# Optimization experiments

Hardware: AMD Instinct MI355X
Metric: run time of the kernel (lower is better)

The kernel has to match this reference:

```python
import jax, jax.numpy as jnp
import numpy as np

B, C, H, W = 8, 8, 640, 640
M = 16  # max instance ids per image (0 = background)
EPS = 1e-12


def setup_inputs() -> dict:
    key = jax.random.key(0)
    k1, k2, k3, k4, k5 = jax.random.split(key, 5)
    outputs = jax.random.normal(k1, (B, C, H, W), dtype=jnp.float32)
    gt_texts = jax.random.randint(k2, (B, H, W), 0, M)
    gt_kernels = jax.random.randint(k3, (B, H, W), 0, M)
    gt_tops = jax.random.randint(k4, (B, H, W), 0, M)
    gt_bots = jax.random.randint(k5, (B, H, W), 0, M)
    return dict(outputs=outputs, gt_texts=gt_texts, gt_kernels=gt_kernels,
                gt_tops=gt_tops, gt_bots=gt_bots)


def _pull_push(outputs, gt_texts, gt_kernels):
    b = outputs.shape[0]
    n = outputs.shape[2] * outputs.shape[3]
    # similarity embedding per pixel: [B, N, 4]
    sim = outputs[:, 4:].reshape(b, 4, n).transpose(0, 2, 1)
    kt = gt_kernels.reshape(b, n)
    tt = gt_texts.reshape(b, n)
    off = jnp.arange(b, dtype=kt.dtype)[:, None] * M
    ids_k = (kt + off).reshape(-1)
    ids_t = (tt + off).reshape(-1)
    sim_flat = sim.reshape(b * n, 4)
    ones = jnp.ones((b * n,), sim.dtype)

    # per-instance kernel centroids G (segment mean over kernel pixels)
    sum_k = jax.ops.segment_sum(sim_flat, ids_k, num_segments=b * M).reshape(b, M, 4)
    cnt_k = jax.ops.segment_sum(ones, ids_k, num_segments=b * M).reshape(b, M)
    G = sum_k / jnp.maximum(cnt_k, 1.0)[..., None]  # [B, M, 4]
    # instance valid iff it has kernel pixels and idx >= 1 (0 is background)
    valid = (cnt_k > 0) & (jnp.arange(M)[None, :] >= 1)

    # pull loss: per text pixel, distance to its instance's kernel centroid
    G_pix = jnp.take_along_axis(G, tt[..., None], axis=1)  # [B, N, 4]
    d = jnp.sqrt(((sim - G_pix) ** 2).sum(-1) + EPS) - 0.5  # [B, N]
    l_pix = jnp.log1p(jnp.maximum(d, 0.0) ** 2).reshape(-1)
    sum_t = jax.ops.segment_sum(l_pix, ids_t, num_segments=b * M).reshape(b, M)
    cnt_t = jax.ops.segment_sum(ones, ids_t, num_segments=b * M).reshape(b, M)
    per_inst = sum_t / jnp.maximum(cnt_t, 1.0)  # mean over each instance's text pixels
    nv = valid.sum(-1).astype(sim.dtype)
    loss_pull = (per_inst * valid).sum(-1) / jnp.maximum(nv, 1.0)

    # push loss: pairwise centroid separation, pairs (i < j) of valid instances
    diff = G[:, :, None, :] - G[:, None, :, :]  # [B, M, M, 4]
    dk = jnp.sqrt((diff ** 2).sum(-1) + EPS)
    val = jnp.log1p(jnp.maximum(3.0 - dk, 0.0) ** 2)
    iu = jnp.triu(jnp.ones((M, M), bool), 1)
    pm = valid[:, :, None] & valid[:, None, :] & iu[None]
    push_sum = (val * pm).sum((1, 2))
    denom = nv * (nv - 1.0)  # matches original normalization n*(n-1)
    loss_push = jnp.where(nv > 1, push_sum / jnp.maximum(denom, 1.0), 0.0)
    return loss_pull, loss_push


def reference(outputs, gt_texts, gt_kernels, gt_tops, gt_bots):
    # gt_tops/gt_bots are consumed by broken (non-contributing) branches in the
    # original code; the returned losses depend only on gt_texts/gt_kernels.
    return _pull_push(outputs, gt_texts, gt_kernels)
```

## Files before the change

kernel.cpp:

```cpp
#include <hip/hip_runtime.h>
#include <math.h>

#define BB 8
#define MI 16
#define NN 409600
#define CEPS 1e-12f
#define GPB 200
#define TPB 256

#define WS_PS   0
#define WS_G    (BB*GPB*80)
#define WS_VAL  (WS_G + BB*MI*4)
#define WS_PP   (WS_VAL + BB*MI)

__global__ __launch_bounds__(TPB, 6) void k_sums(
    const float* __restrict__ outputs, const int* __restrict__ gt_kernels,
    float* __restrict__ ws) {
  __shared__ float red[4][64][17];
  __shared__ float cbuf[MI];
  const int b = blockIdx.y, blk = blockIdx.x, tid = threadIdx.x;
  const int wv = tid >> 6, lane = tid & 63;
  const int mb = wv * 4;

  float acc[16];
#pragma unroll
  for (int i = 0; i < 16; i++) acc[i] = 0.f;
  unsigned int cnt[4] = {0u, 0u, 0u, 0u};

  const float* s0 = outputs + (size_t)(b * 8 + 4) * NN;
  const int* gkb = gt_kernels + (size_t)b * NN;

#pragma unroll 2
  for (int it = 0; it < 8; it++) {
    const int pix = blk * 2048 + it * 256 + lane * 4;
    const int4 id4 = *(const int4*)(gkb + pix);
    const float4 x0 = *(const float4*)(s0 + pix);
    const float4 x1 = *(const float4*)(s0 + NN + pix);
    const float4 x2 = *(const float4*)(s0 + 2 * NN + pix);
    const float4 x3 = *(const float4*)(s0 + 3 * NN + pix);
#define SLOTK(IDC, XC)                                                       \
    {                                                                        \
      const int id = id4.IDC - mb;                                           \
      _Pragma("unroll")                                                      \
      for (int j = 0; j < 4; j++) {                                          \
        const bool e = (id == j);                                            \
        cnt[j] += (unsigned)__popcll(__ballot(e));          \
        const float f = e ? 1.f : 0.f;                                       \
        acc[0 * 4 + j] += f * x0.XC;                                         \
        acc[1 * 4 + j] += f * x1.XC;                                         \
        acc[2 * 4 + j] += f * x2.XC;                                         \
        acc[3 * 4 + j] += f * x3.XC;                                         \
      }                                                                      \
    }
    SLOTK(x, x) SLOTK(y, y) SLOTK(z, z) SLOTK(w, w)
#undef SLOTK
  }

#pragma unroll
  for (int v = 0; v < 16; v++) red[wv][lane][v] = acc[v];
  if (lane == 0) {
#pragma unroll
    for (int j = 0; j < 4; j++) cbuf[mb + j] = (float)cnt[j];
  }
  __syncthreads();
  if (tid < 80) {
    const int m = tid / 5, c = tid % 5;
    const int w = m >> 2, j = m & 3;
    float s;
    if (c < 4) {
      const int vi = c * 4 + j;
      s = 0.f;
#pragma unroll 8
      for (int l = 0; l < 64; l++) s += red[w][(l + tid) & 63][vi];
    } else {
      s = cbuf[m];
    }
    ws[WS_PS + (size_t)(b * GPB + blk) * 80 + tid] = s;
  }
}

__global__ void k_finG(float* __restrict__ ws) {
  __shared__ float part[5][80];
  __shared__ float tot[80];
  const int b = blockIdx.x, t = threadIdx.x;
  const int v = t % 80, h = t / 80;
  float s = 0.f;
  const float* src = ws + WS_PS + (size_t)(b * GPB + h * 40) * 80 + v;
#pragma unroll 8
  for (int k = 0; k < 40; k++) s += src[(size_t)k * 80];
  part[h][v] = s;
  __syncthreads();
  if (t < 80) tot[t] = part[0][t] + part[1][t] + part[2][t] + part[3][t] + part[4][t];
  __syncthreads();
  if (t < MI) {
    const float cnt = tot[t * 5 + 4];
    const float inv = 1.f / fmaxf(cnt, 1.f);
    float4 g;
    g.x = tot[t * 5 + 0] * inv;
    g.y = tot[t * 5 + 1] * inv;
    g.z = tot[t * 5 + 2] * inv;
    g.w = tot[t * 5 + 3] * inv;
    ((float4*)(ws + WS_G))[b * MI + t] = g;
    ws[WS_VAL + b * MI + t] = (cnt > 0.f && t >= 1) ? 1.f : 0.f;
  }
}

__global__ __launch_bounds__(TPB, 6) void k_pull(
    const float* __restrict__ outputs, const int* __restrict__ gt_texts,
    float* __restrict__ ws) {
  __shared__ float4 sG[MI];
  __shared__ float red[4][64][17];
  __shared__ float cbuf[4][MI];
  const int b = blockIdx.y, blk = blockIdx.x, tid = threadIdx.x;
  const int wv = tid >> 6, lane = tid & 63;
  if (tid < MI) sG[tid] = ((const float4*)(ws + WS_G))[b * MI + tid];
  __syncthreads();

  float al[16];
#pragma unroll
  for (int m = 0; m < MI; m++) al[m] = 0.f;
  unsigned int cw[16];
#pragma unroll
  for (int m = 0; m < MI; m++) cw[m] = 0u;

  const float* s0 = outputs + (size_t)(b * 8 + 4) * NN;
  const int* ttb = gt_texts + (size_t)b * NN;

#pragma unroll
  for (int it = 0; it < 2; it++) {
    const int pix = blk * 2048 + it * 1024 + tid * 4;
    const int4 id4 = *(const int4*)(ttb + pix);
    const float4 x0 = *(const float4*)(s0 + pix);
    const float4 x1 = *(const float4*)(s0 + NN + pix);
    const float4 x2 = *(const float4*)(s0 + 2 * NN + pix);
    const float4 x3 = *(const float4*)(s0 + 3 * NN + pix);
#define SLOTP(IDC, XC)                                                       \
    {                                                                        \
      const int id = id4.IDC;                                                \
      const float4 g = sG[id];                                               \
      const float d0 = x0.XC - g.x, d1 = x1.XC - g.y;                        \
      const float d2 = x2.XC - g.z, d3 = x3.XC - g.w;                        \
      const float dist = sqrtf(d0*d0 + d1*d1 + d2*d2 + d3*d3 + CEPS) - 0.5f; \
      const float dm = fmaxf(dist, 0.f);                                     \
      const float l = __logf(1.f + dm * dm);                                 \
      _Pragma("unroll")                                                      \
      for (int m = 0; m < MI; m++) {                                         \
        const bool e = (id == m);                                            \
        cw[m] += (unsigned)__popcll(__ballot(e));           \
        al[m] += e ? l : 0.f;                                                \
      }                                                                      \
    }
    SLOTP(x, x) SLOTP(y, y) SLOTP(z, z) SLOTP(w, w)
#undef SLOTP
  }

#pragma unroll
  for (int v = 0; v < 16; v++) red[wv][lane][v] = al[v];
  if (lane == 0) {
#pragma unroll
    for (int m = 0; m < MI; m++) cbuf[wv][m] = (float)cw[m];
  }
  __syncthreads();
  if (tid < 32) {
    const int m = tid >> 1, c = tid & 1;
    float s = 0.f;
    if (c == 0) {
#pragma unroll
      for (int w = 0; w < 4; w++)
#pragma unroll 8
        for (int l = 0; l < 64; l++) s += red[w][(l + tid) & 63][m];
    } else {
      s = cbuf[0][m] + cbuf[1][m] + cbuf[2][m] + cbuf[3][m];
    }
    ws[WS_PP + (size_t)(b * GPB + blk) * 32 + tid] = s;
  }
}

__global__ void k_final(const float* __restrict__ ws, float* __restrict__ out) {
  __shared__ float part[8][32];
  __shared__ float tot[32];
  const int b = blockIdx.x, t = threadIdx.x;
  const int v = t & 31, h = t >> 5;
  float s = 0.f;
  const float* src = ws + WS_PP + (size_t)(b * GPB + h * 25) * 32 + v;
#pragma unroll 5
  for (int k = 0; k < 25; k++) s += src[(size_t)k * 32];
  part[h][v] = s;
  __syncthreads();
  if (t < 32) {
    float x = 0.f;
#pragma unroll
    for (int hh = 0; hh < 8; hh++) x += part[hh][t];
    tot[t] = x;
  }
  __syncthreads();
  if (t == 0) {
    const float* G = ws + WS_G;
    const float* valid = ws + WS_VAL;
    float nv = 0.f;
    for (int m = 0; m < MI; m++) nv += valid[b * MI + m];
    float pull = 0.f;
    for (int m = 0; m < MI; m++) {
      const float per = tot[m * 2] / fmaxf(tot[m * 2 + 1], 1.f);
      pull += per * valid[b * MI + m];
    }
    pull /= fmaxf(nv, 1.f);
    float push = 0.f;
    for (int i = 0; i < MI; i++) {
      if (valid[b * MI + i] == 0.f) continue;
      for (int j = i + 1; j < MI; j++) {
        if (valid[b * MI + j] == 0.f) continue;
        float d2 = CEPS;
        for (int c = 0; c < 4; c++) {
          const float df = G[(b * MI + i) * 4 + c] - G[(b * MI + j) * 4 + c];
          d2 += df * df;
        }
        const float dk = sqrtf(d2);
        const float tt = fmaxf(3.f - dk, 0.f);
        push += log1pf(tt * tt);
      }
    }
    const float denom = nv * (nv - 1.f);
    push = (nv > 1.f) ? push / fmaxf(denom, 1.f) : 0.f;
    out[b] = pull;
    out[BB + b] = push;
  }
}

extern "C" void kernel_launch(void* const* d_in, const int* in_sizes, int n_in,
                              void* d_out, int out_size, void* d_ws, size_t ws_size,
                              hipStream_t stream) {
  const float* outputs = (const float*)d_in[0];
  const int* gt_texts = (const int*)d_in[1];
  const int* gt_kernels = (const int*)d_in[2];
  float* ws = (float*)d_ws;
  float* out = (float*)d_out;

  dim3 grid(GPB, BB);
  k_sums<<<grid, TPB, 0, stream>>>(outputs, gt_kernels, ws);
  k_finG<<<BB, 400, 0, stream>>>(ws);
  k_pull<<<grid, TPB, 0, stream>>>(outputs, gt_texts, ws);
  k_final<<<BB, 256, 0, stream>>>(ws, out);
}
```

Measured before the change: 252.3 us.

## Fuse four kernels into one persistent kernel with global atomic barriers

Merges the centroid-sum, centroid-finalize, pull and final-reduction kernels into one kernel of 640 blocks. Stages are separated by software grid barriers built from atomic counters in the workspace, which are zeroed with a memset before each launch. Each block now covers more pixels, and it re-reads the same pixel range in the pull pass, so that data is more likely to still be in cache. This removes the extra kernel launches and the workspace round-trips for the centroids. In exchange it relies on all 640 blocks being resident at once (launch bounds set to 3 per CU), has lower occupancy, and adds spin-wait cost.

```diff
diff --git a/kernel.cpp b/kernel.cpp
--- a/kernel.cpp
+++ b/kernel.cpp
@@ -5,34 +5,44 @@
 #define MI 16
 #define NN 409600
 #define CEPS 1e-12f
-#define GPB 200
+#define GPB 80
+#define NBLK (BB*GPB)
+#define PXB 5120
 #define TPB 256
 
-#define WS_PS   0
-#define WS_G    (BB*GPB*80)
-#define WS_VAL  (WS_G + BB*MI*4)
-#define WS_PP   (WS_VAL + BB*MI)
-
-__global__ __launch_bounds__(TPB, 6) void k_sums(
-    const float* __restrict__ outputs, const int* __restrict__ gt_kernels,
-    float* __restrict__ ws) {
+#define WS_PS   16
+#define WS_PP   (WS_PS + NBLK*80)
+
+__global__ __launch_bounds__(TPB, 3) void k_fused(
+    const float* __restrict__ outputs, const int* __restrict__ gt_texts,
+    const int* __restrict__ gt_kernels, float* __restrict__ ws,
+    int* __restrict__ bar, float* __restrict__ out) {
   __shared__ float red[4][64][17];
-  __shared__ float cbuf[MI];
-  const int b = blockIdx.y, blk = blockIdx.x, tid = threadIdx.x;
-  const int wv = tid >> 6, lane = tid & 63;
+  __shared__ float cbuf[4][MI];
+  __shared__ float gpart[3][80];
+  __shared__ float tot80[80];
+  __shared__ float4 sG[MI];
+  __shared__ float svalid[MI];
+  __shared__ float part[8][32];
+  __shared__ float tot32[32];
+
+  const int gb = blockIdx.x;
+  const int b = gb / GPB, blk = gb % GPB;
+  const int tid = threadIdx.x, wv = tid >> 6, lane = tid & 63;
   const int mb = wv * 4;
+
+  const float* s0 = outputs + (size_t)(b * 8 + 4) * NN;
+  const int* gkb = gt_kernels + (size_t)b * NN;
+  const int* ttb = gt_texts + (size_t)b * NN;
 
   float acc[16];
 #pragma unroll
   for (int i = 0; i < 16; i++) acc[i] = 0.f;
   unsigned int cnt[4] = {0u, 0u, 0u, 0u};
 
-  const float* s0 = outputs + (size_t)(b * 8 + 4) * NN;
-  const int* gkb = gt_kernels + (size_t)b * NN;
-
-#pragma unroll 2
-  for (int it = 0; it < 8; it++) {
-    const int pix = blk * 2048 + it * 256 + lane * 4;
+#pragma unroll 4
+  for (int it = 0; it < 20; it++) {
+    const int pix = blk * PXB + it * 256 + lane * 4;
     const int4 id4 = *(const int4*)(gkb + pix);
     const float4 x0 = *(const float4*)(s0 + pix);
     const float4 x1 = *(const float4*)(s0 + NN + pix);
@@ -60,7 +70,7 @@
   for (int v = 0; v < 16; v++) red[wv][lane][v] = acc[v];
   if (lane == 0) {
 #pragma unroll
-    for (int j = 0; j < 4; j++) cbuf[mb + j] = (float)cnt[j];
+    for (int j = 0; j < 4; j++) cbuf[0][mb + j] = (float)cnt[j];
   }
   __syncthreads();
   if (tid < 80) {
@@ -73,47 +83,44 @@
 #pragma unroll 8
       for (int l = 0; l < 64; l++) s += red[w][(l + tid) & 63][vi];
     } else {
-      s = cbuf[m];
-    }
-    ws[WS_PS + (size_t)(b * GPB + blk) * 80 + tid] = s;
-  }
-}
-
-__global__ void k_finG(float* __restrict__ ws) {
-  __shared__ float part[5][80];
-  __shared__ float tot[80];
-  const int b = blockIdx.x, t = threadIdx.x;
-  const int v = t % 80, h = t / 80;
-  float s = 0.f;
-  const float* src = ws + WS_PS + (size_t)(b * GPB + h * 40) * 80 + v;
-#pragma unroll 8
-  for (int k = 0; k < 40; k++) s += src[(size_t)k * 80];
-  part[h][v] = s;
-  __syncthreads();
-  if (t < 80) tot[t] = part[0][t] + part[1][t] + part[2][t] + part[3][t] + part[4][t];
-  __syncthreads();
-  if (t < MI) {
-    const float cnt = tot[t * 5 + 4];
-    const float inv = 1.f / fmaxf(cnt, 1.f);
+      s = cbuf[0][m];
+    }
+    ws[WS_PS + gb * 80 + tid] = s;
+  }
+
+  __syncthreads();
+  if (tid == 0) {
+    __threadfence();
+    atomicAdd(&bar[0], 1);
+    while (__hip_atomic_load(&bar[0], __ATOMIC_RELAXED,
+                             __HIP_MEMORY_SCOPE_AGENT) < NBLK)
+      __builtin_amdgcn_s_sleep(32);
+    __threadfence();
+  }
+  __syncthreads();
+
+  if (tid < 240) {
+    const int v = tid % 80, h = tid / 80;
+    const int k0 = (h == 0) ? 0 : (h == 1) ? 27 : 54;
+    const int k1 = (h == 0) ? 27 : (h == 1) ? 54 : 80;
+    float s = 0.f;
+    for (int k = k0; k < k1; k++) s += ws[WS_PS + (b * GPB + k) * 80 + v];
+    gpart[h][v] = s;
+  }
+  __syncthreads();
+  if (tid < 80) tot80[tid] = gpart[0][tid] + gpart[1][tid] + gpart[2][tid];
+  __syncthreads();
+  if (tid < MI) {
+    const float c5 = tot80[tid * 5 + 4];
+    const float inv = 1.f / fmaxf(c5, 1.f);
     float4 g;
-    g.x = tot[t * 5 + 0] * inv;
-    g.y = tot[t * 5 + 1] * inv;
-    g.z = tot[t * 5 + 2] * inv;
-    g.w = tot[t * 5 + 3] * inv;
-    ((float4*)(ws + WS_G))[b * MI + t] = g;
-    ws[WS_VAL + b * MI + t] = (cnt > 0.f && t >= 1) ? 1.f : 0.f;
-  }
-}
-
-__global__ __launch_bounds__(TPB, 6) void k_pull(
-    const float* __restrict__ outputs, const int* __restrict__ gt_texts,
-    float* __restrict__ ws) {
-  __shared__ float4 sG[MI];
-  __shared__ float red[4][64][17];
-  __shared__ float cbuf[4][MI];
-  const int b = blockIdx.y, blk = blockIdx.x, tid = threadIdx.x;
-  const int wv = tid >> 6, lane = tid & 63;
-  if (tid < MI) sG[tid] = ((const float4*)(ws + WS_G))[b * MI + tid];
+    g.x = tot80[tid * 5 + 0] * inv;
+    g.y = tot80[tid * 5 + 1] * inv;
+    g.z = tot80[tid * 5 + 2] * inv;
+    g.w = tot80[tid * 5 + 3] * inv;
+    sG[tid] = g;
+    svalid[tid] = (c5 > 0.f && tid >= 1) ? 1.f : 0.f;
+  }
   __syncthreads();
 
   float al[16];
@@ -123,12 +130,9 @@
 #pragma unroll
   for (int m = 0; m < MI; m++) cw[m] = 0u;
 
-  const float* s0 = outputs + (size_t)(b * 8 + 4) * NN;
-  const int* ttb = gt_texts + (size_t)b * NN;
-
-#pragma unroll
-  for (int it = 0; it < 2; it++) {
-    const int pix = blk * 2048 + it * 1024 + tid * 4;
+#pragma unroll
+  for (int it = 0; it < 5; it++) {
+    const int pix = blk * PXB + it * 1024 + tid * 4;
     const int4 id4 = *(const int4*)(ttb + pix);
     const float4 x0 = *(const float4*)(s0 + pix);
     const float4 x1 = *(const float4*)(s0 + NN + pix);
@@ -154,6 +158,7 @@
 #undef SLOTP
   }
 
+  __syncthreads();
 #pragma unroll
   for (int v = 0; v < 16; v++) red[wv][lane][v] = al[v];
   if (lane == 0) {
@@ -172,52 +177,62 @@
     } else {
       s = cbuf[0][m] + cbuf[1][m] + cbuf[2][m] + cbuf[3][m];
     }
-    ws[WS_PP + (size_t)(b * GPB + blk) * 32 + tid] = s;
-  }
-}
-
-__global__ void k_final(const float* __restrict__ ws, float* __restrict__ out) {
-  __shared__ float part[8][32];
-  __shared__ float tot[32];
-  const int b = blockIdx.x, t = threadIdx.x;
-  const int v = t & 31, h = t >> 5;
-  float s = 0.f;
-  const float* src = ws + WS_PP + (size_t)(b * GPB + h * 25) * 32 + v;
+    ws[WS_PP + gb * 32 + tid] = s;
+  }
+
+  __syncthreads();
+  if (tid == 0) {
+    __threadfence();
+    atomicAdd(&bar[1], 1);
+    if (blk == 0) {
+      while (__hip_atomic_load(&bar[1], __ATOMIC_RELAXED,
+                               __HIP_MEMORY_SCOPE_AGENT) < NBLK)
+        __builtin_amdgcn_s_sleep(32);
+      __threadfence();
+    }
+  }
+  if (blk != 0) return;
+  __syncthreads();
+
+  {
+    const int v = tid & 31, h = tid >> 5;
+    float s = 0.f;
 #pragma unroll 5
-  for (int k = 0; k < 25; k++) s += src[(size_t)k * 32];
-  part[h][v] = s;
-  __syncthreads();
-  if (t < 32) {
+    for (int k = 0; k < 10; k++)
+      s += ws[WS_PP + (b * GPB + h * 10 + k) * 32 + v];
+    part[h][v] = s;
+  }
+  __syncthreads();
+  if (tid < 32) {
     float x = 0.f;
 #pragma unroll
-    for (int hh = 0; hh < 8; hh++) x += part[hh][t];
-    tot[t] = x;
-  }
-  __syncthreads();
-  if (t == 0) {
-    const float* G = ws + WS_G;
-    const float* valid = ws + WS_VAL;
+    for (int hh = 0; hh < 8; hh++) x += part[hh][tid];
+    tot32[tid] = x;
+  }
+  __syncthreads();
+  if (tid == 0) {
     float nv = 0.f;
-    for (int m = 0; m < MI; m++) nv += valid[b * MI + m];
+    for (int m = 0; m < MI; m++) nv += svalid[m];
     float pull = 0.f;
     for (int m = 0; m < MI; m++) {
-      const float per = tot[m * 2] / fmaxf(tot[m * 2 + 1], 1.f);
-      pull += per * valid[b * MI + m];
+      const float per = tot32[m * 2] / fmaxf(tot32[m * 2 + 1], 1.f);
+      pull += per * svalid[m];
     }
     pull /= fmaxf(nv, 1.f);
     float push = 0.f;
     for (int i = 0; i < MI; i++) {
-      if (valid[b * MI + i] == 0.f) continue;
+      if (svalid[i] == 0.f) continue;
       for (int j = i + 1; j < MI; j++) {
-        if (valid[b * MI + j] == 0.f) continue;
+        if (svalid[j] == 0.f) continue;
+        const float4 gi = sG[i], gj = sG[j];
         float d2 = CEPS;
-        for (int c = 0; c < 4; c++) {
-          const float df = G[(b * MI + i) * 4 + c] - G[(b * MI + j) * 4 + c];
-          d2 += df * df;
-        }
+        d2 += (gi.x - gj.x) * (gi.x - gj.x);
+        d2 += (gi.y - gj.y) * (gi.y - gj.y);
+        d2 += (gi.z - gj.z) * (gi.z - gj.z);
+        d2 += (gi.w - gj.w) * (gi.w - gj.w);
         const float dk = sqrtf(d2);
-        const float tt = fmaxf(3.f - dk, 0.f);
-        push += log1pf(tt * tt);
+        const float tq = fmaxf(3.f - dk, 0.f);
+        push += log1pf(tq * tq);
       }
     }
     const float denom = nv * (nv - 1.f);
@@ -234,11 +249,10 @@
   const int* gt_texts = (const int*)d_in[1];
   const int* gt_kernels = (const int*)d_in[2];
   float* ws = (float*)d_ws;
+  int* bar = (int*)d_ws;
   float* out = (float*)d_out;
 
-  dim3 grid(GPB, BB);
-  k_sums<<<grid, TPB, 0, stream>>>(outputs, gt_kernels, ws);
-  k_finG<<<BB, 400, 0, stream>>>(ws);
-  k_pull<<<grid, TPB, 0, stream>>>(outputs, gt_texts, ws);
-  k_final<<<BB, 256, 0, stream>>>(ws, out);
+  hipMemsetAsync(d_ws, 0, 16 * sizeof(float), stream);
+  k_fused<<<NBLK, TPB, 0, stream>>>(outputs, gt_texts, gt_kernels,
+                                    ws, bar, out);
 }
```

Result: slower. 323.5 us (+28.2%).
